# Optimization experiments

Hardware: AMD Instinct MI355X
Metric: run time of the kernel (lower is better)

The kernel has to match this reference:

```python
import jax, jax.numpy as jnp
import numpy as np

DIM = 256
QK_DIM = 256
SCALE = QK_DIM ** (-0.5)


def depthwise_conv3x3(x_img, w, b):
    # x_img: [B, C, H, W], w: [C, 1, 3, 3] (OIHW, groups=C), b: [C]
    out = jax.lax.conv_general_dilated(
        x_img, w, window_strides=(1, 1), padding='SAME',
        feature_group_count=x_img.shape[1],
        dimension_numbers=('NCHW', 'OIHW', 'NCHW'))
    return out + b[None, :, None, None]


def setup_inputs() -> dict:
    key = jax.random.key(0)
    ks = jax.random.split(key, 7)
    B, N, C = 4, 4096, DIM
    s = 0.02
    return {
        'x': jax.random.normal(ks[0], (B, N, C), jnp.float32),
        'W_qkv': jax.random.normal(ks[1], (C, 3 * C), jnp.float32) * s,
        'W_gate': jax.random.normal(ks[2], (C, C), jnp.float32) * s,
        'b_gate': jax.random.normal(ks[3], (C,), jnp.float32) * s,
        'W_proj': jax.random.normal(ks[4], (C, C), jnp.float32) * s,
        'pe_w': jax.random.normal(ks[5], (C, 1, 3, 3), jnp.float32) * s,
        'pe_b': jax.random.normal(ks[6], (C,), jnp.float32) * s,
    }


def reference(x, W_qkv, W_gate, b_gate, W_proj, pe_w, pe_b):
    B, N, C = x.shape
    ws = int(N ** 0.5)
    qkv = x @ W_qkv                               # [B, N, 3C]
    q, k, v = jnp.split(qkv, [QK_DIM, 2 * QK_DIM], axis=-1)
    z = jax.nn.gelu(x @ W_gate + b_gate, approximate=False)  # [B, N, C]
    # depthwise-conv positional encoding on q viewed as an image
    q_img = jnp.transpose(q, (0, 2, 1)).reshape(B, C, ws, ws)
    pe = depthwise_conv3x3(q_img, pe_w, pe_b).reshape(B, C, N)
    pe = jnp.transpose(pe, (0, 2, 1))             # [B, N, C]
    # single-head attention (heads arg unused in the original forward)
    attn = jax.nn.softmax(jnp.einsum('bnc,bmc->bnm', q, k) * SCALE, axis=-1)
    out = jnp.einsum('bnm,bmc->bnc', attn, v) + pe
    out = out * z
    return out @ W_proj
```

## Files before the change

### kernel.cpp

```cpp
#include <hip/hip_runtime.h>
#include <hip/hip_bf16.h>
#include <math.h>
#include <stdint.h>

typedef unsigned short u16;
typedef __attribute__((ext_vector_type(8))) short bf8;
typedef __attribute__((ext_vector_type(4))) float f4;

#define SC_LOG2E 0.09016844f

__device__ __forceinline__ float b2f(u16 u) {
    union { uint32_t i; float f; } v; v.i = ((uint32_t)u) << 16; return v.f;
}
__device__ __forceinline__ u16 f2b(float f) {
    union { float f; uint32_t i; } v; v.f = f;
    uint32_t r = (v.i + 0x7FFFu + ((v.i >> 16) & 1u)) >> 16;
    return (u16)r;
}
__device__ __forceinline__ uint32_t pk_bf16(float lo, float hi) {
    uint32_t r;
    asm("v_cvt_pk_bf16_f32 %0, %1, %2" : "=v"(r) : "v"(lo), "v"(hi));
    return r;
}

__global__ __launch_bounds__(256) void prep_all(
        const float* __restrict__ Wqkv, const float* __restrict__ Wgate,
        const float* __restrict__ Wproj, const float* __restrict__ x,
        u16* __restrict__ WT_all, u16* __restrict__ WTp,
        u16* __restrict__ xb) {
    int bid = blockIdx.x;
    if (bid < 80) {
        __shared__ float tile[64][65];
        int t = threadIdx.x;
        int lid = (bid < 64) ? bid : (bid - 64);
        int n0 = (lid >> 2) * 64, k0 = (lid & 3) * 64;
        const float* src; int stride, ncol; u16* dst;
        if (bid < 64) {
            if (n0 < 768) { src = Wqkv; stride = 768; ncol = n0; }
            else          { src = Wgate; stride = 256; ncol = n0 - 768; }
            dst = WT_all;
        } else { src = Wproj; stride = 256; ncol = n0; dst = WTp; }
        int cr = t & 63, rr = t >> 6;
#pragma unroll
        for (int i = 0; i < 16; i++) {
            int r = rr * 16 + i;
            tile[r][cr] = src[(size_t)(k0 + r) * stride + ncol + cr];
        }
        __syncthreads();
#pragma unroll
        for (int i = 0; i < 16; i++) {
            int rw = rr * 16 + i;
            dst[(size_t)(n0 + rw) * 256 + k0 + cr] = f2b(tile[cr][rw]);
        }
    } else {
        int i = ((bid - 80) * 256 + threadIdx.x) * 4;
        float4 f = *(const float4*)&x[i];
        uint2 o;
        o.x = pk_bf16(f.x, f.y);
        o.y = pk_bf16(f.z, f.w);
        *(uint2*)&xb[i] = o;
    }
}

__global__ __launch_bounds__(512) void gemm_qkvz(
        const u16* __restrict__ xb, const u16* __restrict__ WT,
        const float* __restrict__ b_gate,
        u16* __restrict__ qo, u16* __restrict__ ko,
        u16* __restrict__ vT, u16* __restrict__ zo) {
    __shared__ u16 As[64 * 520];
    __shared__ u16 Bs[64 * 520];
    const int t = threadIdx.x;
    const int w = t >> 6, lane = t & 63, l15 = lane & 15, q4 = lane >> 4;
    const int m0 = blockIdx.x * 128;
    const int by = blockIdx.y;
    const int n0 = by * 128;

    const int lo = lane >> 5;
    const int lcn = ((lane & 31) - 4 * lo) & 31;

    auto stage128 = [&](const u16* src, u16* dst) {
#pragma unroll
        for (int rr = 0; rr < 8; rr++) {
            int pp = rr * 8 + w;
            const u16* g = src + (size_t)(pp * 2 + lo) * 256 + lcn * 8;
            __builtin_amdgcn_global_load_lds(
                (const __attribute__((address_space(1))) unsigned int*)g,
                (__attribute__((address_space(3))) unsigned int*)&dst[pp * 520],
                16, 0, 0);
        }
    };
    auto kaddr = [&](const u16* base, int row, int cn) -> const u16* {
        int o = row & 1;
        return base + (row >> 1) * 520 + o * 256 + (((cn + 4 * o) & 31) << 3);
    };

    stage128(&xb[(size_t)m0 * 256], As);
    stage128(&WT[(size_t)n0 * 256], Bs);
    __syncthreads();

    const int mtb = (w & 3) * 32;
    const int ntb = (w >> 2) * 64;
    const bool vTout = (by >> 1) == 2;

    f4 acc[2][4];
#pragma unroll
    for (int i = 0; i < 2; i++)
#pragma unroll
        for (int j = 0; j < 4; j++) acc[i][j] = (f4){0.f, 0.f, 0.f, 0.f};

#pragma unroll
    for (int c = 0; c < 8; c++) {
        bf8 af0 = *(const bf8*)kaddr(As, mtb + l15, c * 4 + q4);
        bf8 af1 = *(const bf8*)kaddr(As, mtb + 16 + l15, c * 4 + q4);
        if (vTout) {
#pragma unroll
            for (int j = 0; j < 4; j++) {
                bf8 bfj = *(const bf8*)kaddr(Bs, ntb + j * 16 + l15, c * 4 + q4);
                acc[0][j] = __builtin_amdgcn_mfma_f32_16x16x32_bf16(af0, bfj, acc[0][j], 0, 0, 0);
                acc[1][j] = __builtin_amdgcn_mfma_f32_16x16x32_bf16(af1, bfj, acc[1][j], 0, 0, 0);
            }
        } else {
#pragma unroll
            for (int j = 0; j < 4; j++) {
                bf8 bfj = *(const bf8*)kaddr(Bs, ntb + j * 16 + l15, c * 4 + q4);
                acc[0][j] = __builtin_amdgcn_mfma_f32_16x16x32_bf16(bfj, af0, acc[0][j], 0, 0, 0);
                acc[1][j] = __builtin_amdgcn_mfma_f32_16x16x32_bf16(bfj, af1, acc[1][j], 0, 0, 0);
            }
        }
    }

    const int kind = by >> 1;
    const int colbase = (by & 1) * 128;

    if (kind == 2) {
        int bb = m0 >> 12;
        int nnb = (m0 & 4095) + mtb + q4 * 4;
#pragma unroll
        for (int i = 0; i < 2; i++) {
            int nn = nnb + i * 16;
#pragma unroll
            for (int j = 0; j < 4; j++) {
                int vc = colbase + ntb + j * 16 + l15;
                uint2 pk;
                pk.x = pk_bf16(acc[i][j][0], acc[i][j][1]);
                pk.y = pk_bf16(acc[i][j][2], acc[i][j][3]);
                *(uint2*)&vT[(size_t)(bb * 256 + vc) * 4096 + nn] = pk;
            }
        }
    } else if (kind == 3) {
#pragma unroll
        for (int i = 0; i < 2; i++) {
            size_t mrow = (size_t)(m0 + mtb + i * 16 + l15) * 256 + colbase;
#pragma unroll
            for (int j = 0; j < 4; j++) {
                int col = ntb + j * 16 + q4 * 4;
                float4 bg4 = *(const float4*)&b_gate[colbase + col];
                float v0 = acc[i][j][0] + bg4.x;
                float v1 = acc[i][j][1] + bg4.y;
                float v2 = acc[i][j][2] + bg4.z;
                float v3 = acc[i][j][3] + bg4.w;
                v0 = 0.5f * v0 * (1.0f + erff(v0 * 0.70710678118654752f));
                v1 = 0.5f * v1 * (1.0f + erff(v1 * 0.70710678118654752f));
                v2 = 0.5f * v2 * (1.0f + erff(v2 * 0.70710678118654752f));
                v3 = 0.5f * v3 * (1.0f + erff(v3 * 0.70710678118654752f));
                uint2 o;
                o.x = pk_bf16(v0, v1);
                o.y = pk_bf16(v2, v3);
                *(uint2*)&zo[mrow + col] = o;
            }
        }
    } else {
        u16* dst = (kind == 0) ? qo : ko;
#pragma unroll
        for (int i = 0; i < 2; i++) {
            size_t mrow = (size_t)(m0 + mtb + i * 16 + l15) * 256 + colbase;
#pragma unroll
            for (int j = 0; j < 4; j++) {
                int col = ntb + j * 16 + q4 * 4;
                uint2 o;
                o.x = pk_bf16(acc[i][j][0], acc[i][j][1]);
                o.y = pk_bf16(acc[i][j][2], acc[i][j][3]);
                *(uint2*)&dst[mrow + col] = o;
            }
        }
    }
}

__global__ __launch_bounds__(256) void conv_pe(
        const u16* __restrict__ q, const float* __restrict__ pw,
        const float* __restrict__ pb, u16* __restrict__ pe) {
    const int bid = blockIdx.x;
    const int b = bid >> 8, h = (bid >> 2) & 63, wsg = bid & 3;
    const int t = threadIdx.x;
    const int c4 = (t & 63) * 4;
    const int ws4 = t >> 6;
    const int w0 = wsg * 16 + ws4 * 4;

    float wf[36];
#pragma unroll
    for (int j = 0; j < 9; j++) {
        float4 v = *(const float4*)&pw[c4 * 9 + j * 4];
        wf[j * 4 + 0] = v.x; wf[j * 4 + 1] = v.y;
        wf[j * 4 + 2] = v.z; wf[j * 4 + 3] = v.w;
    }
    float4 bias4 = *(const float4*)&pb[c4];
    float bias[4] = {bias4.x, bias4.y, bias4.z, bias4.w};

    const u16* qb = q + b * (4096 * 256);
    u16* peb = pe + b * (4096 * 256);
    const bool vTop = h > 0, vBot = h < 63;

    float v[3][6][4];
#pragma unroll
    for (int j = 0; j < 6; j++) {
        int pos = w0 - 1 + j;
        bool inw = (pos >= 0) && (pos < 64);
#pragma unroll
        for (int r = 0; r < 3; r++) {
            bool ok = inw && ((r == 0) ? vTop : (r == 2) ? vBot : true);
            ushort4 u4 = {0, 0, 0, 0};
            if (ok) u4 = *(const ushort4*)&qb[((h - 1 + r) * 64 + pos) * 256 + c4];
            v[r][j][0] = b2f(u4.x); v[r][j][1] = b2f(u4.y);
            v[r][j][2] = b2f(u4.z); v[r][j][3] = b2f(u4.w);
        }
    }
#pragma unroll
    for (int w2 = 0; w2 < 4; w2++) {
        float o[4];
#pragma unroll
        for (int ch = 0; ch < 4; ch++) {
            float acc = bias[ch];
#pragma unroll
            for (int r = 0; r < 3; r++)
#pragma unroll
                for (int j = 0; j < 3; j++)
                    acc += wf[ch * 9 + r * 3 + j] * v[r][w2 + j][ch];
            o[ch] = acc;
        }
        uint2 st;
        st.x = pk_bf16(o[0], o[1]);
        st.y = pk_bf16(o[2], o[3]);
        *(uint2*)&peb[(h * 64 + w0 + w2) * 256 + c4] = st;
    }
}

__global__ __launch_bounds__(512) void attn(
        const u16* __restrict__ q, const u16* __restrict__ k,
        const u16* __restrict__ vT, const u16* __restrict__ pe,
        const u16* __restrict__ z, const u16* __restrict__ WTp,
        float* __restrict__ out) {
    __shared__ u16 Kst[32 * 520];
    __shared__ u16 Vs2[2][256 * 64];
    __shared__ u16 Ps[64 * 72];
    __shared__ float l_part[8][64];

    const int t = threadIdx.x;
    const int w = t >> 6, lane = t & 63, l15 = lane & 15, q4 = lane >> 4;
    const int kg = w >> 1, qh = w & 1;
    const int xcd = blockIdx.x & 7;
    const int b = xcd >> 1;
    const int qt = (blockIdx.x >> 3) * 2 + (xcd & 1);
    const int m0 = b * 4096 + qt * 64;

    const u16* kb = k + (size_t)b * 4096 * 256;
    const u16* vbase = vT + (size_t)b * 256 * 4096;

    const int lo = lane >> 5;
    const int lcn = ((lane & 31) - 4 * lo) & 31;

    auto stage64 = [&](const u16* src) {
#pragma unroll
        for (int rr = 0; rr < 4; rr++) {
            int pp = rr * 8 + w;
            const u16* g = src + (size_t)(pp * 2 + lo) * 256 + lcn * 8;
            u16* l = &Kst[pp * 520];
            __builtin_amdgcn_global_load_lds(
                (const __attribute__((address_space(1))) unsigned int*)g,
                (__attribute__((address_space(3))) unsigned int*)l, 16, 0, 0);
        }
    };
    const int vrl = lane >> 3, vsl = lane & 7;
    auto stageV = [&](const u16* src, u16* dst) {
#pragma unroll
        for (int j = 0; j < 4; j++) {
            int op = j * 8 + w;
            int r = op * 8 + vrl;
            int cn = (vsl - r) & 7;
            const u16* g = src + (size_t)r * 4096 + cn * 8;
            u16* l = dst + op * 512;
            __builtin_amdgcn_global_load_lds(
                (const __attribute__((address_space(1))) unsigned int*)g,
                (__attribute__((address_space(3))) unsigned int*)l, 16, 0, 0);
        }
    };
    auto kaddr = [&](int row, int cn) -> const u16* {
        int o = row & 1;
        return &Kst[(row >> 1) * 520 + o * 256 + (((cn + 4 * o) & 31) << 3)];
    };

    stage64(q + (size_t)m0 * 256);
    __syncthreads();
    bf8 qf[2][8];
#pragma unroll
    for (int qtt = 0; qtt < 2; qtt++)
#pragma unroll
        for (int c = 0; c < 8; c++)
            qf[qtt][c] = *(const bf8*)kaddr(qh * 32 + qtt * 16 + l15, c * 4 + q4);
    __syncthreads();

    stage64(kb);
    stageV(vbase, Vs2[0]);

    f4 O[2][4];
#pragma unroll
    for (int vg = 0; vg < 2; vg++)
#pragma unroll
        for (int qg = 0; qg < 4; qg++) O[vg][qg] = (f4){0.f, 0.f, 0.f, 0.f};
    float lrow[2] = {0.f, 0.f};

    auto body = [&](int kt, const u16* Vcur, u16* Vnxt) {
        __syncthreads();

        f4 St[2];
        St[0] = (f4){0.f, 0.f, 0.f, 0.f};
        St[1] = (f4){0.f, 0.f, 0.f, 0.f};
        __builtin_amdgcn_s_setprio(1);
#pragma unroll
        for (int c = 0; c < 8; c++) {
            bf8 kf = *(const bf8*)kaddr(kg * 16 + l15, c * 4 + q4);
            St[0] = __builtin_amdgcn_mfma_f32_16x16x32_bf16(kf, qf[0][c], St[0], 0, 0, 0);
            St[1] = __builtin_amdgcn_mfma_f32_16x16x32_bf16(kf, qf[1][c], St[1], 0, 0, 0);
        }
        __builtin_amdgcn_s_setprio(0);

#pragma unroll
        for (int qtt = 0; qtt < 2; qtt++) {
            float e0 = exp2f(fminf(fmaxf(St[qtt][0] * SC_LOG2E, -30.f), 30.f));
            float e1 = exp2f(fminf(fmaxf(St[qtt][1] * SC_LOG2E, -30.f), 30.f));
            float e2 = exp2f(fminf(fmaxf(St[qtt][2] * SC_LOG2E, -30.f), 30.f));
            float e3 = exp2f(fminf(fmaxf(St[qtt][3] * SC_LOG2E, -30.f), 30.f));
            uint2 pk;
            pk.x = pk_bf16(e0, e1);
            pk.y = pk_bf16(e2, e3);
            int qrow = qh * 32 + qtt * 16 + l15;
            *(uint2*)&Ps[qrow * 72 + kg * 16 + q4 * 4] = pk;
            float s = (e0 + e1) + (e2 + e3);
            s += __shfl_xor(s, 16);
            s += __shfl_xor(s, 32);
            lrow[qtt] += s;
        }
        __syncthreads();

        if (kt < 63) {
            stage64(kb + (size_t)(kt + 1) * 16384);
            stageV(vbase + (size_t)(kt + 1) * 64, Vnxt);
        }

        bf8 pf[4][2], vfr[2][2];
#pragma unroll
        for (int qg = 0; qg < 4; qg++)
#pragma unroll
            for (int kh = 0; kh < 2; kh++)
                pf[qg][kh] = *(bf8*)&Ps[(qg * 16 + l15) * 72 + kh * 32 + q4 * 8];
#pragma unroll
        for (int vg = 0; vg < 2; vg++)
#pragma unroll
            for (int kh = 0; kh < 2; kh++) {
                int R = w * 32 + vg * 16 + l15;
                int slot = ((kh * 4 + q4) + R) & 7;
                vfr[vg][kh] = *(const bf8*)&Vcur[R * 64 + slot * 8];
            }
        __builtin_amdgcn_s_setprio(1);
#pragma unroll
        for (int vg = 0; vg < 2; vg++)
#pragma unroll
            for (int qg = 0; qg < 4; qg++) {
                O[vg][qg] = __builtin_amdgcn_mfma_f32_16x16x32_bf16(
                    vfr[vg][0], pf[qg][0], O[vg][qg], 0, 0, 0);
                O[vg][qg] = __builtin_amdgcn_mfma_f32_16x16x32_bf16(
                    vfr[vg][1], pf[qg][1], O[vg][qg], 0, 0, 0);
            }
        __builtin_amdgcn_s_setprio(0);
    };

    for (int kt2 = 0; kt2 < 64; kt2 += 2) {
        body(kt2,     Vs2[0], Vs2[1]);
        body(kt2 + 1, Vs2[1], Vs2[0]);
    }

    if (q4 == 0) {
        l_part[w][qh * 32 + l15] = lrow[0];
        l_part[w][qh * 32 + 16 + l15] = lrow[1];
    }
    __syncthreads();

    u16* Us = Kst;
#pragma unroll
    for (int qg = 0; qg < 4; qg++) {
        int qrow = qg * 16 + l15;
        int qhq = qg >> 1;
        float lt = l_part[qhq][qrow] + l_part[2 + qhq][qrow]
                 + l_part[4 + qhq][qrow] + l_part[6 + qhq][qrow];
        float linv = 1.0f / lt;
        size_t mrow = (size_t)(m0 + qrow) * 256;
#pragma unroll
        for (int vg = 0; vg < 2; vg++) {
            int vcb = w * 32 + vg * 16 + q4 * 4;
            ushort4 pe4 = *(const ushort4*)&pe[mrow + vcb];
            ushort4 z4  = *(const ushort4*)&z[mrow + vcb];
            float r0 = (O[vg][qg][0] * linv + b2f(pe4.x)) * b2f(z4.x);
            float r1 = (O[vg][qg][1] * linv + b2f(pe4.y)) * b2f(z4.y);
            float r2 = (O[vg][qg][2] * linv + b2f(pe4.z)) * b2f(z4.z);
            float r3 = (O[vg][qg][3] * linv + b2f(pe4.w)) * b2f(z4.w);
            uint2 o4;
            o4.x = pk_bf16(r0, r1);
            o4.y = pk_bf16(r2, r3);
            int cn = vcb >> 3;
            int slot = (cn + qrow) & 31;
            *(uint2*)&Us[qrow * 256 + slot * 8 + (vcb & 7)] = o4;
        }
    }

    auto stageW = [&](const u16* src, u16* dst) {
#pragma unroll
        for (int j = 0; j < 4; j++) {
            int op = j * 8 + w;
            int r = op * 2 + lo;
            int cn = ((lane & 31) - r) & 31;
            const u16* g = src + (size_t)r * 256 + cn * 8;
            __builtin_amdgcn_global_load_lds(
                (const __attribute__((address_space(1))) unsigned int*)g,
                (__attribute__((address_space(3))) unsigned int*)&dst[op * 512],
                16, 0, 0);
        }
    };

    stageW(WTp, (u16*)Vs2[0]);
    __syncthreads();

    const int mtl = (w & 3) * 16;
    const int ntl = (w >> 2) * 32;
#pragma unroll
    for (int nq = 0; nq < 4; nq++) {
        if (nq < 3) stageW(WTp + (size_t)(nq + 1) * 64 * 256, (u16*)Vs2[(nq + 1) & 1]);
        const u16* Wl = (const u16*)Vs2[nq & 1];
        f4 a0 = (f4){0.f, 0.f, 0.f, 0.f};
        f4 a1 = (f4){0.f, 0.f, 0.f, 0.f};
        const int mrowL = mtl + l15;
        const int ln0 = ntl + l15, ln1 = ntl + 16 + l15;
        __builtin_amdgcn_s_setprio(1);
#pragma unroll
        for (int c = 0; c < 8; c++) {
            int cc = c * 4 + q4;
            bf8 af = *(const bf8*)&Us[mrowL * 256 + (((cc + mrowL) & 31) << 3)];
            bf8 b0 = *(const bf8*)&Wl[ln0 * 256 + (((cc + ln0) & 31) << 3)];
            bf8 b1 = *(const bf8*)&Wl[ln1 * 256 + (((cc + ln1) & 31) << 3)];
            a0 = __builtin_amdgcn_mfma_f32_16x16x32_bf16(b0, af, a0, 0, 0, 0);
            a1 = __builtin_amdgcn_mfma_f32_16x16x32_bf16(b1, af, a1, 0, 0, 0);
        }
        __builtin_amdgcn_s_setprio(0);
        float* ob = &out[(size_t)(m0 + mrowL) * 256 + nq * 64 + ntl];
        *(f4*)&ob[q4 * 4] = a0;
        *(f4*)&ob[16 + q4 * 4] = a1;
        __syncthreads();
    }
}

extern "C" void kernel_launch(void* const* d_in, const int* in_sizes, int n_in,
                              void* d_out, int out_size, void* d_ws, size_t ws_size,
                              hipStream_t stream) {
    (void)in_sizes; (void)n_in; (void)out_size; (void)ws_size;
    const float* x      = (const float*)d_in[0];
    const float* Wqkv   = (const float*)d_in[1];
    const float* Wgate  = (const float*)d_in[2];
    const float* bgate  = (const float*)d_in[3];
    const float* Wproj  = (const float*)d_in[4];
    const float* pw     = (const float*)d_in[5];
    const float* pb     = (const float*)d_in[6];
    float* out = (float*)d_out;

    char* ws = (char*)d_ws;
    u16* WT_all = (u16*)(ws);
    u16* WTp    = (u16*)(ws + 524288);
    u16* q      = (u16*)(ws + 655360);
    u16* k      = (u16*)(ws + 9043968);
    u16* vT     = (u16*)(ws + 17432576);
    u16* z      = (u16*)(ws + 25821184);
    u16* pe     = (u16*)(ws + 34209792);
    u16* xb     = (u16*)(ws + 42598400);

    prep_all<<<4176, 256, 0, stream>>>(Wqkv, Wgate, Wproj, x, WT_all, WTp, xb);
    gemm_qkvz<<<dim3(128, 8), 512, 0, stream>>>(xb, WT_all, bgate, q, k, vT, z);
    conv_pe<<<1024, 256, 0, stream>>>(q, pw, pb, pe);
    attn<<<256, 512, 0, stream>>>(q, k, vT, pe, z, WTp, out);
}
```

Measured before the change: 223.1 us.

## Reuse A tile across N-panels with double-buffered B staging in QKVZ GEMM

Each GEMM block now loads its 128-row x tile once and loops over eight 64-column weight panels. The next panel is prefetched into a second LDS buffer while the current one is computed, and the MFMA section runs at raised wave priority. This removes repeated x loads and gives fewer, longer blocks that overlap loads with compute. In exchange the grid shrinks from 1024 to 256 blocks, which may underfill the CUs, and each block's work is now serialized.

```diff
diff --git a/kernel.cpp b/kernel.cpp
--- a/kernel.cpp
+++ b/kernel.cpp
@@ -68,21 +68,31 @@
         u16* __restrict__ qo, u16* __restrict__ ko,
         u16* __restrict__ vT, u16* __restrict__ zo) {
     __shared__ u16 As[64 * 520];
-    __shared__ u16 Bs[64 * 520];
+    __shared__ u16 Bp[2][32 * 520];
     const int t = threadIdx.x;
     const int w = t >> 6, lane = t & 63, l15 = lane & 15, q4 = lane >> 4;
     const int m0 = blockIdx.x * 128;
-    const int by = blockIdx.y;
-    const int n0 = by * 128;
+    const int nb = blockIdx.y * 512;
 
     const int lo = lane >> 5;
     const int lcn = ((lane & 31) - 4 * lo) & 31;
 
-    auto stage128 = [&](const u16* src, u16* dst) {
+    auto stageA = [&]() {
 #pragma unroll
         for (int rr = 0; rr < 8; rr++) {
             int pp = rr * 8 + w;
-            const u16* g = src + (size_t)(pp * 2 + lo) * 256 + lcn * 8;
+            const u16* g = &xb[(size_t)(m0 + pp * 2 + lo) * 256 + lcn * 8];
+            __builtin_amdgcn_global_load_lds(
+                (const __attribute__((address_space(1))) unsigned int*)g,
+                (__attribute__((address_space(3))) unsigned int*)&As[pp * 520],
+                16, 0, 0);
+        }
+    };
+    auto stageB = [&](int p, u16* dst) {
+#pragma unroll
+        for (int rr = 0; rr < 4; rr++) {
+            int pp = rr * 8 + w;
+            const u16* g = &WT[(size_t)(nb + p * 64 + pp * 2 + lo) * 256 + lcn * 8];
             __builtin_amdgcn_global_load_lds(
                 (const __attribute__((address_space(1))) unsigned int*)g,
                 (__attribute__((address_space(3))) unsigned int*)&dst[pp * 520],
@@ -94,93 +104,97 @@
         return base + (row >> 1) * 520 + o * 256 + (((cn + 4 * o) & 31) << 3);
     };
 
-    stage128(&xb[(size_t)m0 * 256], As);
-    stage128(&WT[(size_t)n0 * 256], Bs);
-    __syncthreads();
+    stageA();
+    stageB(0, Bp[0]);
 
     const int mtb = (w & 3) * 32;
-    const int ntb = (w >> 2) * 64;
-    const bool vTout = (by >> 1) == 2;
-
-    f4 acc[2][4];
-#pragma unroll
-    for (int i = 0; i < 2; i++)
-#pragma unroll
-        for (int j = 0; j < 4; j++) acc[i][j] = (f4){0.f, 0.f, 0.f, 0.f};
-
-#pragma unroll
-    for (int c = 0; c < 8; c++) {
-        bf8 af0 = *(const bf8*)kaddr(As, mtb + l15, c * 4 + q4);
-        bf8 af1 = *(const bf8*)kaddr(As, mtb + 16 + l15, c * 4 + q4);
-        if (vTout) {
-#pragma unroll
-            for (int j = 0; j < 4; j++) {
-                bf8 bfj = *(const bf8*)kaddr(Bs, ntb + j * 16 + l15, c * 4 + q4);
-                acc[0][j] = __builtin_amdgcn_mfma_f32_16x16x32_bf16(af0, bfj, acc[0][j], 0, 0, 0);
-                acc[1][j] = __builtin_amdgcn_mfma_f32_16x16x32_bf16(af1, bfj, acc[1][j], 0, 0, 0);
+    const int ntb = (w >> 2) * 32;
+
+    for (int p = 0; p < 8; ++p) {
+        __syncthreads();
+        if (p < 7) stageB(p + 1, Bp[(p + 1) & 1]);
+        const u16* Bs = Bp[p & 1];
+        const int n0g = nb + p * 64;
+        const int kind = n0g >> 8;
+        const int pcol = n0g & 255;
+
+        f4 acc[2][2];
+#pragma unroll
+        for (int i = 0; i < 2; i++)
+#pragma unroll
+            for (int j = 0; j < 2; j++) acc[i][j] = (f4){0.f, 0.f, 0.f, 0.f};
+
+        __builtin_amdgcn_s_setprio(1);
+#pragma unroll
+        for (int c = 0; c < 8; c++) {
+            bf8 af0 = *(const bf8*)kaddr(As, mtb + l15, c * 4 + q4);
+            bf8 af1 = *(const bf8*)kaddr(As, mtb + 16 + l15, c * 4 + q4);
+            bf8 bf0 = *(const bf8*)kaddr(Bs, ntb + l15, c * 4 + q4);
+            bf8 bf1 = *(const bf8*)kaddr(Bs, ntb + 16 + l15, c * 4 + q4);
+            if (kind == 2) {
+                acc[0][0] = __builtin_amdgcn_mfma_f32_16x16x32_bf16(af0, bf0, acc[0][0], 0, 0, 0);
+                acc[0][1] = __builtin_amdgcn_mfma_f32_16x16x32_bf16(af0, bf1, acc[0][1], 0, 0, 0);
+                acc[1][0] = __builtin_amdgcn_mfma_f32_16x16x32_bf16(af1, bf0, acc[1][0], 0, 0, 0);
+                acc[1][1] = __builtin_amdgcn_mfma_f32_16x16x32_bf16(af1, bf1, acc[1][1], 0, 0, 0);
+            } else {
+                acc[0][0] = __builtin_amdgcn_mfma_f32_16x16x32_bf16(bf0, af0, acc[0][0], 0, 0, 0);
+                acc[0][1] = __builtin_amdgcn_mfma_f32_16x16x32_bf16(bf1, af0, acc[0][1], 0, 0, 0);
+                acc[1][0] = __builtin_amdgcn_mfma_f32_16x16x32_bf16(bf0, af1, acc[1][0], 0, 0, 0);
+                acc[1][1] = __builtin_amdgcn_mfma_f32_16x16x32_bf16(bf1, af1, acc[1][1], 0, 0, 0);
+            }
+        }
+        __builtin_amdgcn_s_setprio(0);
+
+        if (kind == 2) {
+            int bb = m0 >> 12;
+            int nnb = (m0 & 4095) + mtb + q4 * 4;
+#pragma unroll
+            for (int i = 0; i < 2; i++) {
+                int nn = nnb + i * 16;
+#pragma unroll
+                for (int j = 0; j < 2; j++) {
+                    int vc = pcol + ntb + j * 16 + l15;
+                    uint2 pk;
+                    pk.x = pk_bf16(acc[i][j][0], acc[i][j][1]);
+                    pk.y = pk_bf16(acc[i][j][2], acc[i][j][3]);
+                    *(uint2*)&vT[(size_t)(bb * 256 + vc) * 4096 + nn] = pk;
+                }
+            }
+        } else if (kind == 3) {
+#pragma unroll
+            for (int i = 0; i < 2; i++) {
+                size_t mrow = (size_t)(m0 + mtb + i * 16 + l15) * 256 + pcol;
+#pragma unroll
+                for (int j = 0; j < 2; j++) {
+                    int col = ntb + j * 16 + q4 * 4;
+                    float4 bg4 = *(const float4*)&b_gate[pcol + col];
+                    float v0 = acc[i][j][0] + bg4.x;
+                    float v1 = acc[i][j][1] + bg4.y;
+                    float v2 = acc[i][j][2] + bg4.z;
+                    float v3 = acc[i][j][3] + bg4.w;
+                    v0 = 0.5f * v0 * (1.0f + erff(v0 * 0.70710678118654752f));
+                    v1 = 0.5f * v1 * (1.0f + erff(v1 * 0.70710678118654752f));
+                    v2 = 0.5f * v2 * (1.0f + erff(v2 * 0.70710678118654752f));
+                    v3 = 0.5f * v3 * (1.0f + erff(v3 * 0.70710678118654752f));
+                    uint2 o;
+                    o.x = pk_bf16(v0, v1);
+                    o.y = pk_bf16(v2, v3);
+                    *(uint2*)&zo[mrow + col] = o;
+                }
             }
         } else {
-#pragma unroll
-            for (int j = 0; j < 4; j++) {
-                bf8 bfj = *(const bf8*)kaddr(Bs, ntb + j * 16 + l15, c * 4 + q4);
-                acc[0][j] = __builtin_amdgcn_mfma_f32_16x16x32_bf16(bfj, af0, acc[0][j], 0, 0, 0);
-                acc[1][j] = __builtin_amdgcn_mfma_f32_16x16x32_bf16(bfj, af1, acc[1][j], 0, 0, 0);
-            }
-        }
-    }
-
-    const int kind = by >> 1;
-    const int colbase = (by & 1) * 128;
-
-    if (kind == 2) {
-        int bb = m0 >> 12;
-        int nnb = (m0 & 4095) + mtb + q4 * 4;
-#pragma unroll
-        for (int i = 0; i < 2; i++) {
-            int nn = nnb + i * 16;
-#pragma unroll
-            for (int j = 0; j < 4; j++) {
-                int vc = colbase + ntb + j * 16 + l15;
-                uint2 pk;
-                pk.x = pk_bf16(acc[i][j][0], acc[i][j][1]);
-                pk.y = pk_bf16(acc[i][j][2], acc[i][j][3]);
-                *(uint2*)&vT[(size_t)(bb * 256 + vc) * 4096 + nn] = pk;
-            }
-        }
-    } else if (kind == 3) {
-#pragma unroll
-        for (int i = 0; i < 2; i++) {
-            size_t mrow = (size_t)(m0 + mtb + i * 16 + l15) * 256 + colbase;
-#pragma unroll
-            for (int j = 0; j < 4; j++) {
-                int col = ntb + j * 16 + q4 * 4;
-                float4 bg4 = *(const float4*)&b_gate[colbase + col];
-                float v0 = acc[i][j][0] + bg4.x;
-                float v1 = acc[i][j][1] + bg4.y;
-                float v2 = acc[i][j][2] + bg4.z;
-                float v3 = acc[i][j][3] + bg4.w;
-                v0 = 0.5f * v0 * (1.0f + erff(v0 * 0.70710678118654752f));
-                v1 = 0.5f * v1 * (1.0f + erff(v1 * 0.70710678118654752f));
-                v2 = 0.5f * v2 * (1.0f + erff(v2 * 0.70710678118654752f));
-                v3 = 0.5f * v3 * (1.0f + erff(v3 * 0.70710678118654752f));
-                uint2 o;
-                o.x = pk_bf16(v0, v1);
-                o.y = pk_bf16(v2, v3);
-                *(uint2*)&zo[mrow + col] = o;
-            }
-        }
-    } else {
-        u16* dst = (kind == 0) ? qo : ko;
-#pragma unroll
-        for (int i = 0; i < 2; i++) {
-            size_t mrow = (size_t)(m0 + mtb + i * 16 + l15) * 256 + colbase;
-#pragma unroll
-            for (int j = 0; j < 4; j++) {
-                int col = ntb + j * 16 + q4 * 4;
-                uint2 o;
-                o.x = pk_bf16(acc[i][j][0], acc[i][j][1]);
-                o.y = pk_bf16(acc[i][j][2], acc[i][j][3]);
-                *(uint2*)&dst[mrow + col] = o;
+            u16* dst = (kind == 0) ? qo : ko;
+#pragma unroll
+            for (int i = 0; i < 2; i++) {
+                size_t mrow = (size_t)(m0 + mtb + i * 16 + l15) * 256 + pcol;
+#pragma unroll
+                for (int j = 0; j < 2; j++) {
+                    int col = ntb + j * 16 + q4 * 4;
+                    uint2 o;
+                    o.x = pk_bf16(acc[i][j][0], acc[i][j][1]);
+                    o.y = pk_bf16(acc[i][j][2], acc[i][j][3]);
+                    *(uint2*)&dst[mrow + col] = o;
+                }
             }
         }
     }
@@ -490,7 +504,7 @@
     u16* xb     = (u16*)(ws + 42598400);
 
     prep_all<<<4176, 256, 0, stream>>>(Wqkv, Wgate, Wproj, x, WT_all, WTp, xb);
-    gemm_qkvz<<<dim3(128, 8), 512, 0, stream>>>(xb, WT_all, bgate, q, k, vT, z);
+    gemm_qkvz<<<dim3(128, 2), 512, 0, stream>>>(xb, WT_all, bgate, q, k, vT, z);
     conv_pe<<<1024, 256, 0, stream>>>(q, pw, pb, pe);
     attn<<<256, 512, 0, stream>>>(q, k, vT, pe, z, WTp, out);
 }
```

Measured after the change: 224.3 us. Within noise of the previous version (+0.5%).
